# Kernel tuning notes

Hardware: AMD Instinct MI355X
Metric: run time of the kernel (lower is better)

## Reference

```python
import jax, jax.numpy as jnp
import numpy as np

NUM_HEADS = 8
EPS = 1e-12  # torch F.normalize eps


def _l2norm(t):
    n = jnp.linalg.norm(t, axis=-1, keepdims=True)
    return t / jnp.maximum(n, EPS)


def setup_inputs() -> dict:
    key = jax.random.key(0)
    k1, k2, k3 = jax.random.split(key, 3)
    B, T, N, D = 16, 12, 1024, 128
    x = jax.random.normal(k1, (B, T, N, D), dtype=jnp.float32)
    # Linear(model_dim, 3*model_dim, bias=False): stored as (D, 3D) for x @ W
    W_qkv = jax.random.normal(k2, (D, 3 * D), dtype=jnp.float32) * (1.0 / np.sqrt(D))
    W_out = jax.random.normal(k3, (D, D), dtype=jnp.float32) * (1.0 / np.sqrt(D))
    b_out = jnp.zeros((D,), dtype=jnp.float32)
    return {"x": x, "W_qkv": W_qkv, "W_out": W_out, "b_out": b_out}


def reference(x, W_qkv, W_out, b_out):
    B, T, N, D = x.shape
    H = NUM_HEADS
    hd = D // H
    qkv = x @ W_qkv                                  # (B,T,N,3D)
    q, k, v = jnp.split(qkv, 3, axis=-1)
    # split heads + flatten (B,T) -> b = B*T, matching torch stack/flatten
    qs = _l2norm(q.reshape(B * T, N, H, hd))          # (b,N,H,m)
    ks = _l2norm(k.reshape(B * T, N, H, hd))
    vs = v.reshape(B * T, N, H, hd)
    # linear attention: running kv sum + normalizer
    kvs = jnp.einsum('blhm,blhd->bhmd', ks, vs)       # (b,H,m,d)
    attn_num = jnp.einsum('bnhm,bhmd->bnhd', qs, kvs) + N * vs
    ks_sum = jnp.sum(ks, axis=1)                      # (b,H,m)
    normalizer = jnp.einsum('bnhm,bhm->bnh', qs, ks_sum)[..., None] + N
    out = attn_num / normalizer                       # (b,N,H,d)
    out = out.reshape(B, T, N, D)
    return out @ W_out + b_out
```

## Files before the change

### kernel.cpp

```cpp
#include <hip/hip_runtime.h>
#include <hip/hip_bf16.h>

#define NBATCH 192
#define SEQ    1024
#define DIM    128
#define NH     8
#define EPS    1e-12f

typedef short bf16x8 __attribute__((ext_vector_type(8)));
typedef float f32x4  __attribute__((ext_vector_type(4)));

#define KVSP_F   1572864
#define KSSUM_F  24576
#define WSWT_OFF ((size_t)(KVSP_F + KSSUM_F) * 4)

static __device__ __forceinline__ unsigned short f2bf(float f) {
    unsigned u = __builtin_bit_cast(unsigned, f);
    u += 0x7fff + ((u >> 16) & 1);
    return (unsigned short)(u >> 16);
}

static __device__ __forceinline__ unsigned pk2(float a, float b) {
    __hip_bfloat162 h = __float22bfloat162_rn(make_float2(a, b));
    unsigned r;
    __builtin_memcpy(&r, &h, 4);
    return r;
}
static __device__ __forceinline__ unsigned short bf1(float a) {
    __hip_bfloat16 h = __float2bfloat16(a);
    unsigned short r;
    __builtin_memcpy(&r, &h, 2);
    return r;
}

template <int CTRL>
static __device__ __forceinline__ float dpp_add(float v) {
    int j = __builtin_amdgcn_mov_dpp(__builtin_bit_cast(int, v), CTRL, 0xf, 0xf, false);
    return v + __builtin_bit_cast(float, j);
}
static __device__ __forceinline__ float r16sum(float v) {
    v = dpp_add<0xB1>(v);
    v = dpp_add<0x4E>(v);
    v = dpp_add<0x141>(v);
    v = dpp_add<0x140>(v);
    return v;
}

static __device__ __forceinline__ int strip_addr(int row, int el) {
    return row * 32 + ((((el >> 3) ^ (row & 3)) << 3) | (el & 7));
}

static __device__ __forceinline__ uint2 pack4(float a, float b, float c, float d) {
    uint2 r;
    r.x = pk2(a, b);
    r.y = pk2(c, d);
    return r;
}

static __device__ __forceinline__ bf16x8 cvt8(float4 a, float4 b) {
    uint4 u;
    u.x = pk2(a.x, a.y); u.y = pk2(a.z, a.w);
    u.z = pk2(b.x, b.y); u.w = pk2(b.z, b.w);
    return __builtin_bit_cast(bf16x8, u);
}

static __device__ __forceinline__ bf16x8 gfrag(const unsigned short* __restrict__ wT,
                                               int ct, int ks, int lane) {
    return *reinterpret_cast<const bf16x8*>(wT + ((ct * 4 + ks) * 64 + lane) * 8);
}

__global__ __launch_bounds__(256) void k0_prep(const float* __restrict__ Wqkv,
                                               const float* __restrict__ Wout,
                                               float* __restrict__ kssum_ws,
                                               unsigned short* __restrict__ wsWT) {
    int i = blockIdx.x * 256 + threadIdx.x;
    if (i < KSSUM_F) kssum_ws[i] = 0.0f;
    int which = i >> 14, e = i & 16383;
    int j = e & 7, f = e >> 3;
    int n15 = f & 15, q = (f >> 4) & 3, ks = (f >> 6) & 3, ct = f >> 8;
    int k = ks * 32 + q * 8 + j, n = ct * 16 + n15;
    float v = (which < 3) ? Wqkv[k * 384 + which * 128 + n] : Wout[k * 128 + n];
    wsWT[i] = f2bf(v);
}

__global__ __launch_bounds__(512, 4) void k1_kv(const float* __restrict__ x,
                                                const unsigned short* __restrict__ wsWT,
                                                float* __restrict__ kvs_part,
                                                float* __restrict__ kssum_ws) {
    __shared__ float redf[16384];
    __shared__ unsigned short strips[8192];
    int t = threadIdx.x, w = t >> 6, lane = t & 63, q = lane >> 4, n15 = lane & 15;
    int b = blockIdx.x >> 2, seg = blockIdx.x & 3;
    const unsigned short* wkT = wsWT + 16384;
    const unsigned short* wvT = wsWT + 32768;
    unsigned short* knS = strips + w * 1024;
    unsigned short* vS  = knS + 512;

    bf16x8 ah[2][4];
#pragma unroll
    for (int rs = 0; rs < 2; ++rs) {
        int row = seg * 256 + w * 32 + rs * 16 + n15;
        const float* xr = x + (size_t)(b * SEQ + row) * DIM;
#pragma unroll
        for (int ks = 0; ks < 4; ++ks) {
            float4 p0 = *reinterpret_cast<const float4*>(xr + ks * 32 + q * 8);
            float4 p1 = *reinterpret_cast<const float4*>(xr + ks * 32 + q * 8 + 4);
            ah[rs][ks] = cvt8(p0, p1);
        }
    }

#pragma unroll 1
    for (int ct = 0; ct < 8; ++ct) {
        f32x4 ka[2] = {(f32x4){0,0,0,0}, (f32x4){0,0,0,0}};
        f32x4 va[2] = {(f32x4){0,0,0,0}, (f32x4){0,0,0,0}};
#pragma unroll
        for (int ks = 0; ks < 4; ++ks) {
            bf16x8 kb = gfrag(wkT, ct, ks, lane);
            bf16x8 vb = gfrag(wvT, ct, ks, lane);
#pragma unroll
            for (int rs = 0; rs < 2; ++rs) {
                ka[rs] = __builtin_amdgcn_mfma_f32_16x16x32_bf16(ah[rs][ks], kb, ka[rs], 0, 0, 0);
                va[rs] = __builtin_amdgcn_mfma_f32_16x16x32_bf16(ah[rs][ks], vb, va[rs], 0, 0, 0);
            }
        }
        float ksum = 0.f;
#pragma unroll
        for (int rs = 0; rs < 2; ++rs) {
            float kn[4];
#pragma unroll
            for (int r = 0; r < 4; ++r) {
                float val = ka[rs][r];
                float ssq = r16sum(val * val);
                float di  = 1.0f / fmaxf(sqrtf(ssq), EPS);
                kn[r] = val * di;
                ksum += kn[r];
            }
            *reinterpret_cast<uint2*>(knS + strip_addr(n15, rs * 16 + q * 4)) =
                pack4(kn[0], kn[1], kn[2], kn[3]);
            *reinterpret_cast<uint2*>(vS + strip_addr(n15, rs * 16 + q * 4)) =
                pack4(va[rs][0], va[rs][1], va[rs][2], va[rs][3]);
        }
        bf16x8 aK = *reinterpret_cast<const bf16x8*>(knS + strip_addr(n15, q * 8));
        bf16x8 bV = *reinterpret_cast<const bf16x8*>(vS + strip_addr(n15, q * 8));
        f32x4 kacc = __builtin_amdgcn_mfma_f32_16x16x32_bf16(aK, bV, (f32x4){0,0,0,0}, 0, 0, 0);
#pragma unroll
        for (int r = 0; r < 4; ++r)
            redf[w * 2048 + ct * 256 + (q * 4 + r) * 16 + n15] = kacc[r];
        float s = ksum;
        s += __shfl_xor(s, 16); s += __shfl_xor(s, 32);
        if (lane < 16) atomicAdd(&kssum_ws[b * 128 + ct * 16 + n15], s);
    }

    __syncthreads();
    float* myPart = kvs_part + (size_t)blockIdx.x * 2048;
#pragma unroll
    for (int i = 0; i < 4; ++i) {
        int el = i * 512 + t;
        float s = 0.f;
#pragma unroll
        for (int ww = 0; ww < 8; ++ww) s += redf[ww * 2048 + el];
        myPart[el] = s;
    }
}

__global__ __launch_bounds__(512, 4) void k2_out(const float* __restrict__ x,
                                                 const unsigned short* __restrict__ wsWT,
                                                 const float* __restrict__ kvs_part,
                                                 const float* __restrict__ kssum_ws,
                                                 const float* __restrict__ Wqkv,
                                                 const float* __restrict__ bout,
                                                 float* __restrict__ out) {
    __shared__ unsigned short lds[26624];
    unsigned short* kvsT   = lds;
    unsigned short* strips = lds + 4096;
    unsigned short* uLds   = lds + 8192;
    unsigned short* tile   = lds + 10240;
    int t = threadIdx.x, w = t >> 6, lane = t & 63, q = lane >> 4, n15 = lane & 15;
    int b = blockIdx.x >> 2, seg = blockIdx.x & 3, rowbase = seg * 256;
    const unsigned short* wqT = wsWT;
    const unsigned short* wvT = wsWT + 32768;
    const unsigned short* woT = wsWT + 49152;

    {
        int row = t >> 2, part = t & 3, h = row >> 4, d = row & 15;
        const float* kp = kvs_part + (size_t)b * 4 * 2048;
        unsigned es[8];
#pragma unroll
        for (int j = 0; j < 8; j += 2) {
            int m0 = part * 8 + j;
            float lo = 0.f, hi = 0.f;
#pragma unroll
            for (int s = 0; s < 4; ++s) {
                if (m0     < 16) lo += kp[s * 2048 + h * 256 + m0 * 16 + d];
                if (m0 + 1 < 16) hi += kp[s * 2048 + h * 256 + (m0 + 1) * 16 + d];
            }
            es[j] = pk2(lo, hi);
        }
        uint4 v = {es[0], es[2], es[4], es[6]};
        *reinterpret_cast<uint4*>(kvsT + row * 32 + ((part ^ (row & 3)) << 3)) = v;
    }

    {
#pragma unroll
        for (int p4 = 0; p4 < 4; ++p4) {
            int p = t * 4 + p4;
            int c = p >> 4, h = p & 15;
            float u = 0.f;
            if (h < 8) {
                const float* wr = Wqkv + c * 384 + h * 16;
                const float* ks = kssum_ws + b * 128 + h * 16;
#pragma unroll
                for (int m = 0; m < 16; ++m) u += wr[m] * ks[m];
            }
            uLds[(((c >> 5) * 4 + ((c >> 3) & 3)) * 16 + h) * 8 + (c & 7)] = bf1(u);
        }
    }

    unsigned short* myS = strips + w * 512;
    unsigned short* tw  = tile + w * 2048;
    {
        uint2 z = {0, 0};
        *reinterpret_cast<uint2*>(myS + strip_addr(n15, 16 + q * 4)) = z;
    }
    __syncthreads();

#pragma unroll 1
    for (int rs = 0; rs < 2; ++rs) {
        bf16x8 ahc[4];
        {
            int row = rowbase + w * 32 + rs * 16 + n15;
            const float* xr = x + (size_t)(b * SEQ + row) * DIM;
#pragma unroll
            for (int ks = 0; ks < 4; ++ks) {
                float4 p0 = *reinterpret_cast<const float4*>(xr + ks * 32 + q * 8);
                float4 p1 = *reinterpret_cast<const float4*>(xr + ks * 32 + q * 8 + 4);
                ahc[ks] = cvt8(p0, p1);
            }
        }
        f32x4 ttC = (f32x4){0,0,0,0};
#pragma unroll
        for (int ks = 0; ks < 4; ++ks) {
            bf16x8 uf = *reinterpret_cast<const bf16x8*>(uLds + (ks * 64 + lane) * 8);
            ttC = __builtin_amdgcn_mfma_f32_16x16x32_bf16(ahc[ks], uf, ttC, 0, 0, 0);
        }

#pragma unroll 1
        for (int h = 0; h < 8; ++h) {
            f32x4 qa = (f32x4){0,0,0,0};
            f32x4 va = (f32x4){0,0,0,0};
#pragma unroll
            for (int ks = 0; ks < 4; ++ks) {
                bf16x8 qb = gfrag(wqT, h, ks, lane);
                bf16x8 vb = gfrag(wvT, h, ks, lane);
                qa = __builtin_amdgcn_mfma_f32_16x16x32_bf16(ahc[ks], qb, qa, 0, 0, 0);
                va = __builtin_amdgcn_mfma_f32_16x16x32_bf16(ahc[ks], vb, va, 0, 0, 0);
            }
            int srcl = (lane & 48) | h;
            float pv[4];
#pragma unroll
            for (int r = 0; r < 4; ++r) {
                float val = qa[r];
                float ssq = r16sum(val * val);
                float tt  = __shfl(ttC[r], srcl);
                float di  = 1.0f / fmaxf(sqrtf(ssq), EPS);
                float inv = 1.0f / (tt * di + (float)SEQ);
                pv[r] = val * di * inv;
                va[r] *= (float)SEQ * inv;
            }
#pragma unroll
            for (int r = 0; r < 4; ++r)
                myS[strip_addr(q * 4 + r, n15)] = bf1(pv[r]);
            bf16x8 aq = *reinterpret_cast<const bf16x8*>(myS + strip_addr(n15, q * 8));
            bf16x8 bk = *reinterpret_cast<const bf16x8*>(kvsT + strip_addr(h * 16 + n15, q * 8));
            va = __builtin_amdgcn_mfma_f32_16x16x32_bf16(aq, bk, va, 0, 0, 0);
#pragma unroll
            for (int r = 0; r < 4; ++r) {
                int rt = q * 4 + r;
                int colg = h * 2 + (n15 >> 3);
                tw[rt * 128 + (((colg ^ rt) << 3) | (n15 & 7))] = bf1(va[r]);
            }
        }

        bf16x8 ap[4];
#pragma unroll
        for (int ks = 0; ks < 4; ++ks)
            ap[ks] = *reinterpret_cast<const bf16x8*>(
                tw + n15 * 128 + ((((ks << 2) + q) ^ n15) << 3));
#pragma unroll 1
        for (int ct = 0; ct < 8; ++ct) {
            f32x4 oa = (f32x4){0,0,0,0};
#pragma unroll
            for (int ks = 0; ks < 4; ++ks) {
                bf16x8 bb = gfrag(woT, ct, ks, lane);
                oa = __builtin_amdgcn_mfma_f32_16x16x32_bf16(ap[ks], bb, oa, 0, 0, 0);
            }
            float bo = bout[ct * 16 + n15];
#pragma unroll
            for (int r = 0; r < 4; ++r) {
                int row = rowbase + w * 32 + rs * 16 + q * 4 + r;
                out[(size_t)(b * SEQ + row) * DIM + ct * 16 + n15] = oa[r] + bo;
            }
        }
    }
}

extern "C" void kernel_launch(void* const* d_in, const int* in_sizes, int n_in,
                              void* d_out, int out_size, void* d_ws, size_t ws_size,
                              hipStream_t stream) {
    const float* x    = (const float*)d_in[0];
    const float* Wqkv = (const float*)d_in[1];
    const float* Wout = (const float*)d_in[2];
    const float* bout = (const float*)d_in[3];
    float* out = (float*)d_out;

    float* kvs_part = (float*)d_ws;
    float* kssum_ws = kvs_part + KVSP_F;
    unsigned short* wsWT = (unsigned short*)((char*)d_ws + WSWT_OFF);

    k0_prep<<<dim3(256), dim3(256), 0, stream>>>(Wqkv, Wout, kssum_ws, wsWT);
    k1_kv<<<dim3(768), dim3(512), 0, stream>>>(x, wsWT, kvs_part, kssum_ws);
    k2_out<<<dim3(768), dim3(512), 0, stream>>>(x, wsWT, kvs_part, kssum_ws, Wqkv, bout, out);
}
```

Before: 297.4 us.

## Compute normalizer from raw q via MFMA with ks_sum instead of precomputed W·ks_sum

Drops the per-block precomputation of U = Wq·ks_sum, which read Wqkv from global memory, and the extra MFMA that turned it into the normalizer term. The raw q tile is now staged to LDS once, and two MFMAs against the ks_sum fragment and the kv tile give both q·ks_sum and q·kvs. L2 normalization and the normalizer division are applied afterwards in the epilogue. This removes global Wqkv reads and the shuffle, shrinks LDS use and reorders the q/v MFMA chains. It adds one more MFMA per head and changes bf16 rounding, since unnormalized q is now quantized.

```diff
diff --git a/kernel.cpp b/kernel.cpp
--- a/kernel.cpp
+++ b/kernel.cpp
@@ -167,14 +167,13 @@
                                                  const unsigned short* __restrict__ wsWT,
                                                  const float* __restrict__ kvs_part,
                                                  const float* __restrict__ kssum_ws,
-                                                 const float* __restrict__ Wqkv,
                                                  const float* __restrict__ bout,
                                                  float* __restrict__ out) {
-    __shared__ unsigned short lds[26624];
+    __shared__ unsigned short lds[25088];
     unsigned short* kvsT   = lds;
     unsigned short* strips = lds + 4096;
-    unsigned short* uLds   = lds + 8192;
-    unsigned short* tile   = lds + 10240;
+    unsigned short* kssF   = lds + 8192;
+    unsigned short* tile   = lds + 8704;
     int t = threadIdx.x, w = t >> 6, lane = t & 63, q = lane >> 4, n15 = lane & 15;
     int b = blockIdx.x >> 2, seg = blockIdx.x & 3, rowbase = seg * 256;
     const unsigned short* wqT = wsWT;
@@ -199,21 +198,9 @@
         uint4 v = {es[0], es[2], es[4], es[6]};
         *reinterpret_cast<uint4*>(kvsT + row * 32 + ((part ^ (row & 3)) << 3)) = v;
     }
-
-    {
-#pragma unroll
-        for (int p4 = 0; p4 < 4; ++p4) {
-            int p = t * 4 + p4;
-            int c = p >> 4, h = p & 15;
-            float u = 0.f;
-            if (h < 8) {
-                const float* wr = Wqkv + c * 384 + h * 16;
-                const float* ks = kssum_ws + b * 128 + h * 16;
-#pragma unroll
-                for (int m = 0; m < 16; ++m) u += wr[m] * ks[m];
-            }
-            uLds[(((c >> 5) * 4 + ((c >> 3) & 3)) * 16 + h) * 8 + (c & 7)] = bf1(u);
-        }
+    if (t < 256) {
+        int h = t >> 5, k = t & 31;
+        kssF[t] = (k < 16) ? bf1(kssum_ws[b * 128 + h * 16 + k]) : (unsigned short)0;
     }
 
     unsigned short* myS = strips + w * 512;
@@ -237,47 +224,39 @@
                 ahc[ks] = cvt8(p0, p1);
             }
         }
-        f32x4 ttC = (f32x4){0,0,0,0};
-#pragma unroll
-        for (int ks = 0; ks < 4; ++ks) {
-            bf16x8 uf = *reinterpret_cast<const bf16x8*>(uLds + (ks * 64 + lane) * 8);
-            ttC = __builtin_amdgcn_mfma_f32_16x16x32_bf16(ahc[ks], uf, ttC, 0, 0, 0);
-        }
 
 #pragma unroll 1
         for (int h = 0; h < 8; ++h) {
             f32x4 qa = (f32x4){0,0,0,0};
-            f32x4 va = (f32x4){0,0,0,0};
 #pragma unroll
             for (int ks = 0; ks < 4; ++ks) {
                 bf16x8 qb = gfrag(wqT, h, ks, lane);
+                qa = __builtin_amdgcn_mfma_f32_16x16x32_bf16(ahc[ks], qb, qa, 0, 0, 0);
+            }
+#pragma unroll
+            for (int r = 0; r < 4; ++r)
+                myS[strip_addr(q * 4 + r, n15)] = bf1(qa[r]);
+            f32x4 va = (f32x4){0,0,0,0};
+#pragma unroll
+            for (int ks = 0; ks < 4; ++ks) {
                 bf16x8 vb = gfrag(wvT, h, ks, lane);
-                qa = __builtin_amdgcn_mfma_f32_16x16x32_bf16(ahc[ks], qb, qa, 0, 0, 0);
                 va = __builtin_amdgcn_mfma_f32_16x16x32_bf16(ahc[ks], vb, va, 0, 0, 0);
             }
-            int srcl = (lane & 48) | h;
-            float pv[4];
+            bf16x8 aqr = *reinterpret_cast<const bf16x8*>(myS + strip_addr(n15, q * 8));
+            bf16x8 kf  = *reinterpret_cast<const bf16x8*>(kssF + h * 32 + q * 8);
+            f32x4 tt4 = __builtin_amdgcn_mfma_f32_16x16x32_bf16(aqr, kf, (f32x4){0,0,0,0}, 0, 0, 0);
+            bf16x8 bk = *reinterpret_cast<const bf16x8*>(kvsT + strip_addr(h * 16 + n15, q * 8));
+            f32x4 rn  = __builtin_amdgcn_mfma_f32_16x16x32_bf16(aqr, bk, (f32x4){0,0,0,0}, 0, 0, 0);
 #pragma unroll
             for (int r = 0; r < 4; ++r) {
                 float val = qa[r];
                 float ssq = r16sum(val * val);
-                float tt  = __shfl(ttC[r], srcl);
                 float di  = 1.0f / fmaxf(sqrtf(ssq), EPS);
-                float inv = 1.0f / (tt * di + (float)SEQ);
-                pv[r] = val * di * inv;
-                va[r] *= (float)SEQ * inv;
-            }
-#pragma unroll
-            for (int r = 0; r < 4; ++r)
-                myS[strip_addr(q * 4 + r, n15)] = bf1(pv[r]);
-            bf16x8 aq = *reinterpret_cast<const bf16x8*>(myS + strip_addr(n15, q * 8));
-            bf16x8 bk = *reinterpret_cast<const bf16x8*>(kvsT + strip_addr(h * 16 + n15, q * 8));
-            va = __builtin_amdgcn_mfma_f32_16x16x32_bf16(aq, bk, va, 0, 0, 0);
-#pragma unroll
-            for (int r = 0; r < 4; ++r) {
+                float inv = 1.0f / (tt4[r] * di + (float)SEQ);
+                float pre = rn[r] * di * inv + va[r] * (float)SEQ * inv;
                 int rt = q * 4 + r;
                 int colg = h * 2 + (n15 >> 3);
-                tw[rt * 128 + (((colg ^ rt) << 3) | (n15 & 7))] = bf1(va[r]);
+                tw[rt * 128 + (((colg ^ rt) << 3) | (n15 & 7))] = bf1(pre);
             }
         }
 
@@ -319,5 +298,5 @@
 
     k0_prep<<<dim3(256), dim3(256), 0, stream>>>(Wqkv, Wout, kssum_ws, wsWT);
     k1_kv<<<dim3(768), dim3(512), 0, stream>>>(x, wsWT, kvs_part, kssum_ws);
-    k2_out<<<dim3(768), dim3(512), 0, stream>>>(x, wsWT, kvs_part, kssum_ws, Wqkv, bout, out);
-}
+    k2_out<<<dim3(768), dim3(512), 0, stream>>>(x, wsWT, kvs_part, kssum_ws, bout, out);
+}
```

Result: faster. 285.0 us (-4.2%).
